# Optimization experiments

Measured on AMD Instinct MI355X. Metric: run time of the kernel, lower is better.

Reference implementation:

```python
import jax, jax.numpy as jnp
import numpy as np

DIM = 128
HID = 128
EPS = 1e-6  # flax nnx.LayerNorm default epsilon


def _layernorm(x, scale, bias):
    mu = jnp.mean(x, axis=-1, keepdims=True)
    var = jnp.mean(jnp.square(x - mu), axis=-1, keepdims=True)
    return (x - mu) * jax.lax.rsqrt(var + EPS) * scale + bias


def setup_inputs() -> dict:
    key = jax.random.key(0)
    ks = jax.random.split(key, 16)
    B, N = 1, 512
    s = 1.0 / np.sqrt(DIM)
    inp = {
        "x": jax.random.normal(ks[0], (B, N, N, DIM), dtype=jnp.float32),
        "src_mask": jnp.ones((B, N), dtype=jnp.float32),
        "norm_scale": jnp.ones((DIM,), jnp.float32),
        "norm_bias": jnp.zeros((DIM,), jnp.float32),
        "W_left": jax.random.normal(ks[1], (DIM, HID), jnp.float32) * s,
        "b_left": jnp.zeros((HID,), jnp.float32),
        "W_right": jax.random.normal(ks[2], (DIM, HID), jnp.float32) * s,
        "b_right": jnp.zeros((HID,), jnp.float32),
        "W_lgate": jax.random.normal(ks[3], (DIM, HID), jnp.float32) * s,
        "b_lgate": jnp.zeros((HID,), jnp.float32),
        "W_rgate": jax.random.normal(ks[4], (DIM, HID), jnp.float32) * s,
        "b_rgate": jnp.zeros((HID,), jnp.float32),
        "W_ogate": jax.random.normal(ks[5], (DIM, HID), jnp.float32) * s,
        "b_ogate": jnp.zeros((HID,), jnp.float32),
        "out_norm_scale": jnp.ones((HID,), jnp.float32),
        "out_norm_bias": jnp.zeros((HID,), jnp.float32),
        "W_out": jax.random.normal(ks[6], (HID, DIM), jnp.float32) * (1.0 / np.sqrt(HID)),
        "b_out": jnp.zeros((DIM,), jnp.float32),
    }
    return inp


def reference(x, src_mask, norm_scale, norm_bias, W_left, b_left, W_right, b_right,
              W_lgate, b_lgate, W_rgate, b_rgate, W_ogate, b_ogate,
              out_norm_scale, out_norm_bias, W_out, b_out):
    # pair mask [B,N,N,1] = outer product of token mask
    m = src_mask.astype(jnp.float32)
    mask = (m[:, :, None] * m[:, None, :])[..., None]

    xn = _layernorm(x, norm_scale, norm_bias)  # [B,N,N,D]

    left = (xn @ W_left + b_left) * mask
    right = (xn @ W_right + b_right) * mask
    left = left * jax.nn.sigmoid(xn @ W_lgate + b_lgate)
    right = right * jax.nn.sigmoid(xn @ W_rgate + b_rgate)
    out_gate = jax.nn.sigmoid(xn @ W_ogate + b_ogate)

    # ingoing mix: '... k i d, ... k j d -> ... i j d'
    out = jnp.einsum('bkid,bkjd->bijd', left, right)

    out = _layernorm(out, out_norm_scale, out_norm_bias) * out_gate
    return out @ W_out + b_out
```

## Files before the change

### kernel.cpp

```cpp
#include <hip/hip_runtime.h>


#define NN 512
#define DD 128
#define PT (NN * NN)

typedef float f4 __attribute__((ext_vector_type(4)));
typedef __bf16 bf8 __attribute__((ext_vector_type(8)));
typedef unsigned short u16;
typedef unsigned int u32;
typedef u16 us4 __attribute__((ext_vector_type(4)));
typedef u16 us8 __attribute__((ext_vector_type(8)));

__device__ __forceinline__ u16 f2bf(float f) {
    u32 u = __float_as_uint(f);
    return (u16)((u + 0x7fffu + ((u >> 16) & 1u)) >> 16);
}
__device__ __forceinline__ float bf2f(u16 h) { return __uint_as_float(((u32)h) << 16); }
__device__ __forceinline__ float sigm(float x) {
    return __builtin_amdgcn_rcpf(1.0f + __builtin_amdgcn_exp2f(-1.4426950408889634f * x));
}
__device__ __forceinline__ f4 mfma16(bf8 a, bf8 b, f4 c) {
    return __builtin_amdgcn_mfma_f32_16x16x32_bf16(a, b, c, 0, 0, 0);
}
__device__ __forceinline__ void async16(u16* lds, const u16* g) {
    __builtin_amdgcn_global_load_lds((const __attribute__((address_space(1))) u32*)(const void*)g,
                                     (__attribute__((address_space(3))) u32*)(void*)lds, 16, 0, 0);
}

__global__ __launch_bounds__(256) void kW(const float* __restrict__ wlg, const float* __restrict__ wl,
                                          const float* __restrict__ wrg, const float* __restrict__ wr,
                                          const float* __restrict__ wog, const float* __restrict__ wout,
                                          u16* __restrict__ wt, u16* __restrict__ wtout) {
    __shared__ float tile[128 * 129];
    const float* srcs[6] = {wlg, wl, wrg, wr, wog, wout};
    const int b = blockIdx.x;
    const float* s = srcs[b];
    u16* dst = (b < 5) ? (wt + b * 16384) : wtout;
    const int t = threadIdx.x;
    for (int idx = t; idx < 16384; idx += 256) {
        int k = idx >> 7, n = idx & 127;
        tile[k * 129 + n] = s[idx];
    }
    __syncthreads();
    for (int idx = t; idx < 16384; idx += 256) {
        int n = idx >> 7, k = idx & 127;
        dst[n * 128 + k] = f2bf(tile[k * 129 + n]);
    }
}

__global__ __launch_bounds__(256) void kA(const float* __restrict__ x, const float* __restrict__ smask,
                                          const float* __restrict__ nsc, const float* __restrict__ nbi,
                                          const float* __restrict__ b_l, const float* __restrict__ b_r,
                                          const float* __restrict__ b_lg, const float* __restrict__ b_rg,
                                          const float* __restrict__ b_og, const u16* __restrict__ wt,
                                          u16* __restrict__ left_v, u16* __restrict__ right_v,
                                          u16* __restrict__ gate) {
    __shared__ u16 xs[128 * 136];
    __shared__ float ns[128], nb[128], smk[128];
    u16* tmp = xs;

    const int t = threadIdx.x;
    const int bid = blockIdx.x;
    const int i_blk = bid & 511;
    const int k0 = (bid >> 9) << 7;

    if (t < 128) { ns[t] = nsc[t]; nb[t] = nbi[t]; smk[t] = smask[k0 + t]; }
    const float mi = smask[i_blk];
    __syncthreads();

    {
        const int rr = t >> 1, h = t & 1;
        const float* xr = x + ((long)(k0 + rr) * NN + i_blk) * DD + h * 64;
        f4 xv[16];
#pragma unroll
        for (int q = 0; q < 16; ++q) xv[q] = ((const f4*)xr)[q];
        float s = 0.f, ss = 0.f;
#pragma unroll
        for (int q = 0; q < 16; ++q)
#pragma unroll
            for (int e = 0; e < 4; ++e) { float f = xv[q][e]; s += f; ss += f * f; }
        s += __shfl_xor(s, 1); ss += __shfl_xor(ss, 1);
        const float mu = s * (1.f / 128.f);
        const float rstd = rsqrtf(ss * (1.f / 128.f) - mu * mu + 1e-6f);
        u16* xrow = xs + rr * 136 + h * 64;
#pragma unroll
        for (int q = 0; q < 16; ++q) {
            f4 sc = ((const f4*)ns)[h * 16 + q];
            f4 bi = ((const f4*)nb)[h * 16 + q];
            us4 pk;
#pragma unroll
            for (int e = 0; e < 4; ++e) pk[e] = f2bf((xv[q][e] - mu) * rstd * sc[e] + bi[e]);
            *(us4*)(xrow + q * 4) = pk;
        }
    }
    __syncthreads();

    const int lane = t & 63, w = t >> 6;
    const int m = lane & 15, q = lane >> 4;

    bf8 af[2][4];
#pragma unroll
    for (int st = 0; st < 2; ++st) {
        const int row = (w * 2 + st) * 16 + m;
#pragma unroll
        for (int kc = 0; kc < 4; ++kc) af[st][kc] = *(const bf8*)&xs[row * 136 + kc * 32 + q * 8];
    }
    __syncthreads();

#pragma unroll
    for (int g = 0; g < 3; ++g) {
        const u16* wg = wt + (g == 0 ? 0 : (g == 1 ? 2 * 16384 : 4 * 16384));
        const float* bg = (g == 0) ? b_lg : (g == 1 ? b_rg : b_og);
        f4 accG[16];
#pragma unroll
        for (int nt = 0; nt < 8; ++nt) {
            bf8 bfr[4];
#pragma unroll
            for (int kc = 0; kc < 4; ++kc)
                bfr[kc] = *(const bf8*)(wg + (nt * 16 + m) * 128 + kc * 32 + q * 8);
#pragma unroll
            for (int st = 0; st < 2; ++st) {
                f4 a = {0.f, 0.f, 0.f, 0.f};
#pragma unroll
                for (int kc = 0; kc < 4; ++kc) a = mfma16(af[st][kc], bfr[kc], a);
                accG[nt * 2 + st] = a;
            }
        }
        if (g < 2) {
            const u16* wv = wt + (g == 0 ? 1 : 3) * 16384;
            const float* bv = (g == 0) ? b_l : b_r;
#pragma unroll
            for (int nt = 0; nt < 8; ++nt) {
                bf8 bfr[4];
#pragma unroll
                for (int kc = 0; kc < 4; ++kc)
                    bfr[kc] = *(const bf8*)(wv + (nt * 16 + m) * 128 + kc * 32 + q * 8);
                const int d = nt * 16 + m;
                const float bvn = bv[d], bgn = bg[d];
#pragma unroll
                for (int st = 0; st < 2; ++st) {
                    f4 a = {0.f, 0.f, 0.f, 0.f};
#pragma unroll
                    for (int kc = 0; kc < 4; ++kc) a = mfma16(af[st][kc], bfr[kc], a);
                    const int rr0 = (w * 2 + st) * 16 + q * 4;
                    us4 pk;
#pragma unroll
                    for (int r = 0; r < 4; ++r) {
                        float gv = sigm(accG[nt * 2 + st][r] + bgn);
                        pk[r] = f2bf((a[r] + bvn) * (smk[rr0 + r] * mi) * gv);
                    }
                    *(us4*)&tmp[d * 136 + rr0] = pk;
                }
            }
        } else {
#pragma unroll
            for (int nt = 0; nt < 8; ++nt) {
                const int d = nt * 16 + m;
                const float bgn = bg[d];
#pragma unroll
                for (int st = 0; st < 2; ++st) {
                    const int rr0 = (w * 2 + st) * 16 + q * 4;
#pragma unroll
                    for (int r = 0; r < 4; ++r)
                        tmp[(rr0 + r) * 136 + d] = f2bf(sigm(accG[nt * 2 + st][r] + bgn));
                }
            }
        }
        __syncthreads();
        if (g < 2) {
            u16* dst = (g == 0) ? left_v : right_v;
#pragma unroll
            for (int r8 = 0; r8 < 8; ++r8) {
                const int d = (t >> 4) + r8 * 16;
                const int mc = t & 15;
                us8 vv = *(const us8*)&tmp[d * 136 + mc * 8];
                *(us8*)(dst + (long)d * PT + (long)i_blk * NN + k0 + mc * 8) = vv;
            }
        } else {
#pragma unroll
            for (int r8 = 0; r8 < 8; ++r8) {
                const int rrr = (t >> 4) + r8 * 16;
                const int dc = t & 15;
                us8 vv = *(const us8*)&tmp[rrr * 136 + dc * 8];
                *(us8*)(gate + ((long)(k0 + rrr) * NN + i_blk) * DD + dc * 8) = vv;
            }
        }
        __syncthreads();
    }
}

__global__ __launch_bounds__(256) void kB(const u16* __restrict__ left_v, const u16* __restrict__ right_v,
                                          u16* __restrict__ out_t) {
    __shared__ u16 smem[128 * 136];
    u16* As = smem;
    u16* Bs = smem + 4096;
    const int t = threadIdx.x, lane = t & 63, w = t >> 6;
    const int bid = blockIdx.x;
    const int d = bid >> 4;
    const int ti = (bid & 3) * 128;
    const int tj = ((bid >> 2) & 3) * 128;
    const long dbase = (long)d * PT;
    const int frow = lane >> 2;
    const int fc = (lane & 3) ^ ((lane >> 3) & 3);
    const int m = lane & 15, q = lane >> 4;
    const int sl = q ^ ((m >> 1) & 3);
    const int mrow0 = (w & 1) * 64;
    const int nrow0 = (w >> 1) * 64;

    f4 zero = {0.f, 0.f, 0.f, 0.f};
    f4 acc[16];
#pragma unroll
    for (int z = 0; z < 16; ++z) acc[z] = zero;

    const u16* Agb = left_v + dbase + (long)ti * NN;
    const u16* Bgb = right_v + dbase + (long)tj * NN;

    for (int ks = 0; ks < 16; ++ks) {
        __syncthreads();
#pragma unroll
        for (int inst = 0; inst < 2; ++inst) {
            const int rbase = w * 32 + inst * 16;
            const int row = rbase + frow;
            async16(As + rbase * 32, Agb + (long)row * NN + ks * 32 + fc * 8);
            async16(Bs + rbase * 32, Bgb + (long)row * NN + ks * 32 + fc * 8);
        }
        __syncthreads();
        bf8 af[4], bfv[4];
#pragma unroll
        for (int mt = 0; mt < 4; ++mt) af[mt] = *(const bf8*)&As[(mrow0 + mt * 16 + m) * 32 + sl * 8];
#pragma unroll
        for (int nt = 0; nt < 4; ++nt) bfv[nt] = *(const bf8*)&Bs[(nrow0 + nt * 16 + m) * 32 + sl * 8];
#pragma unroll
        for (int mt = 0; mt < 4; ++mt)
#pragma unroll
            for (int nt = 0; nt < 4; ++nt) acc[mt * 4 + nt] = mfma16(af[mt], bfv[nt], acc[mt * 4 + nt]);
    }
    __syncthreads();
    u16* ct = smem;
#pragma unroll
    for (int mt = 0; mt < 4; ++mt)
#pragma unroll
        for (int nt = 0; nt < 4; ++nt) {
            const int row0 = mrow0 + mt * 16 + q * 4;
            const int col = nrow0 + nt * 16 + m;
            f4 a = acc[mt * 4 + nt];
#pragma unroll
            for (int r = 0; r < 4; ++r) ct[(row0 + r) * 136 + col] = f2bf(a[r]);
        }
    __syncthreads();
#pragma unroll
    for (int r8 = 0; r8 < 8; ++r8) {
        const int row = (t >> 4) + r8 * 16;
        const int mc = t & 15;
        us8 vv = *(const us8*)&ct[row * 136 + mc * 8];
        *(us8*)(out_t + dbase + (long)(ti + row) * NN + tj + mc * 8) = vv;
    }
}

__global__ __launch_bounds__(256) void kC(const u16* __restrict__ out_t, const u16* __restrict__ gate,
                                          const float* __restrict__ osc_g, const float* __restrict__ obi_g,
                                          const u16* __restrict__ wtout, const float* __restrict__ b_out,
                                          float* __restrict__ out) {
    __shared__ u16 os[128 * 128];
    __shared__ float osc[128], obi[128];
    const int t = threadIdx.x;
    const int bid = blockIdx.x;
    const int i = bid >> 2;
    const int j0 = (bid & 3) * 128;
    if (t < 128) { osc[t] = osc_g[t]; obi[t] = obi_g[t]; }
    const long p0 = (long)i * NN + j0;

#pragma unroll
    for (int r8 = 0; r8 < 8; ++r8) {
        const int dd = (t >> 4) + r8 * 16;
        const int mm = t & 15;
        us8 vv = *(const us8*)(out_t + (long)dd * PT + (long)i * NN + j0 + mm * 8);
        const int cd = dd >> 3, dl = dd & 7;
#pragma unroll
        for (int e = 0; e < 8; ++e) {
            const int ee = e ^ (mm & 7);
            const int j = mm * 8 + ee;
            os[j * 128 + ((cd ^ (j & 15)) << 3) + dl] = vv[ee];
        }
    }
    __syncthreads();
    {
        const int j = t >> 1, h = t & 1;
        const long p = p0 + j;
        float s = 0.f, ss = 0.f;
#pragma unroll
        for (int cc = 0; cc < 8; ++cc) {
            const int cd = h * 8 + cc;
            us8 vv = *(const us8*)&os[j * 128 + ((cd ^ (j & 15)) << 3)];
#pragma unroll
            for (int e = 0; e < 8; ++e) { float f = bf2f(vv[e]); s += f; ss += f * f; }
        }
        s += __shfl_xor(s, 1); ss += __shfl_xor(ss, 1);
        const float mu = s * (1.f / 128.f);
        const float rstd = rsqrtf(ss * (1.f / 128.f) - mu * mu + 1e-6f);
#pragma unroll
        for (int cc = 0; cc < 8; ++cc) {
            const int cd = h * 8 + cc;
            u16* slotp = &os[j * 128 + ((cd ^ (j & 15)) << 3)];
            us8 vv = *(const us8*)slotp;
            us8 gv = *(const us8*)(gate + p * DD + cd * 8);
            us8 rv;
#pragma unroll
            for (int e = 0; e < 8; ++e) {
                const int d2 = cd * 8 + e;
                float f = (bf2f(vv[e]) - mu) * rstd * osc[d2] + obi[d2];
                rv[e] = f2bf(f * bf2f(gv[e]));
            }
            *(us8*)slotp = rv;
        }
    }
    __syncthreads();
    const int lane = t & 63, w = t >> 6;
    const int m = lane & 15, q = lane >> 4;
    bf8 af[2][4];
#pragma unroll
    for (int st = 0; st < 2; ++st) {
        const int jr = (w * 2 + st) * 16 + m;
#pragma unroll
        for (int kc = 0; kc < 4; ++kc) {
            const int cd = kc * 4 + q;
            af[st][kc] = *(const bf8*)&os[jr * 128 + ((cd ^ (jr & 15)) << 3)];
        }
    }
#pragma unroll
    for (int nt = 0; nt < 8; ++nt) {
        bf8 bfr[4];
#pragma unroll
        for (int kc = 0; kc < 4; ++kc)
            bfr[kc] = *(const bf8*)(wtout + (nt * 16 + m) * 128 + kc * 32 + q * 8);
        const float bo = b_out[nt * 16 + m];
#pragma unroll
        for (int st = 0; st < 2; ++st) {
            f4 a = {0.f, 0.f, 0.f, 0.f};
#pragma unroll
            for (int kc = 0; kc < 4; ++kc) a = mfma16(af[st][kc], bfr[kc], a);
            const int rr0 = (w * 2 + st) * 16 + q * 4;
#pragma unroll
            for (int r = 0; r < 4; ++r) out[(p0 + rr0 + r) * DD + nt * 16 + m] = a[r] + bo;
        }
    }
}

extern "C" void kernel_launch(void* const* d_in, const int* in_sizes, int n_in, void* d_out, int out_size,
                              void* d_ws, size_t ws_size, hipStream_t stream) {
    const float* x = (const float*)d_in[0];
    const float* sm = (const float*)d_in[1];
    const float* nsc = (const float*)d_in[2];
    const float* nbi = (const float*)d_in[3];
    const float* wl = (const float*)d_in[4];
    const float* bl = (const float*)d_in[5];
    const float* wr = (const float*)d_in[6];
    const float* br = (const float*)d_in[7];
    const float* wlg = (const float*)d_in[8];
    const float* blg = (const float*)d_in[9];
    const float* wrg = (const float*)d_in[10];
    const float* brg = (const float*)d_in[11];
    const float* wog = (const float*)d_in[12];
    const float* bog = (const float*)d_in[13];
    const float* onsc = (const float*)d_in[14];
    const float* onbi = (const float*)d_in[15];
    const float* wout = (const float*)d_in[16];
    const float* bout = (const float*)d_in[17];

    char* ws = (char*)d_ws;
    u16* wt = (u16*)ws;
    u16* wtout = (u16*)(ws + 163840);
    u16* left_v = (u16*)(ws + 262144);
    u16* right_v = left_v + (long)DD * PT;
    u16* gate = right_v + (long)DD * PT;
    u16* out_t = gate + (long)DD * PT;

    kW<<<6, 256, 0, stream>>>(wlg, wl, wrg, wr, wog, wout, wt, wtout);
    kA<<<2048, 256, 0, stream>>>(x, sm, nsc, nbi, bl, br, blg, brg, bog, wt, left_v, right_v, gate);
    kB<<<2048, 256, 0, stream>>>(left_v, right_v, out_t);
    kC<<<2048, 256, 0, stream>>>(out_t, gate, onsc, onbi, wtout, bout, (float*)d_out);
}
```

Measured before the change: 582.4 us.

## Stage LayerNorm input via async global-to-LDS loads and build MFMA fragments directly

Each wave loads its x rows into swizzled fp32 LDS staging with async 16-byte copies, in two 16-row rounds. It computes LayerNorm stats with 4 lanes per row and writes the normalized bf16 A-fragments straight into registers. This drops the bf16 LDS round trip and one barrier, and it hides global latency behind async copies. The cost is a serialized second load round per wave, plus extra shuffles and waitcnt handling.

Result: no change. 575.8 us (-1.1%).

```diff
diff --git a/kernel.cpp b/kernel.cpp
--- a/kernel.cpp
+++ b/kernel.cpp
@@ -59,52 +59,77 @@
     __shared__ u16 xs[128 * 136];
     __shared__ float ns[128], nb[128], smk[128];
     u16* tmp = xs;
+    float* stg = (float*)xs;
 
     const int t = threadIdx.x;
     const int bid = blockIdx.x;
     const int i_blk = bid & 511;
     const int k0 = (bid >> 9) << 7;
+    const int lane = t & 63, w = t >> 6;
+    const int m = lane & 15, q = lane >> 4;
 
     if (t < 128) { ns[t] = nsc[t]; nb[t] = nbi[t]; smk[t] = smask[k0 + t]; }
     const float mi = smask[i_blk];
-    __syncthreads();
-
-    {
-        const int rr = t >> 1, h = t & 1;
-        const float* xr = x + ((long)(k0 + rr) * NN + i_blk) * DD + h * 64;
-        f4 xv[16];
-#pragma unroll
-        for (int q = 0; q < 16; ++q) xv[q] = ((const f4*)xr)[q];
+
+#pragma unroll
+    for (int it = 0; it < 8; ++it) {
+        const int rl = it * 2 + (lane >> 5);
+        const int c = (lane & 31) ^ (rl & 7);
+        const float* gp = x + ((long)(k0 + w * 32 + rl) * NN + i_blk) * DD + c * 4;
+        async16((u16*)(stg + w * 2048 + it * 256), (const u16*)gp);
+    }
+
+    bf8 af[2][4];
+#pragma unroll
+    for (int rd = 0; rd < 2; ++rd) {
+        if (rd == 0) {
+            __syncthreads();
+        } else {
+            asm volatile("s_waitcnt lgkmcnt(0)" ::: "memory");
+            __builtin_amdgcn_sched_barrier(0);
+#pragma unroll
+            for (int it = 0; it < 8; ++it) {
+                const int rl = it * 2 + (lane >> 5);
+                const int c = (lane & 31) ^ (rl & 7);
+                const float* gp = x + ((long)(k0 + w * 32 + 16 + rl) * NN + i_blk) * DD + c * 4;
+                async16((u16*)(stg + w * 2048 + it * 256), (const u16*)gp);
+            }
+            asm volatile("s_waitcnt vmcnt(0)" ::: "memory");
+            __builtin_amdgcn_sched_barrier(0);
+        }
+        const float* wbase = stg + w * 2048;
+        const int rl_s = lane >> 2, h2 = lane & 3;
         float s = 0.f, ss = 0.f;
-#pragma unroll
-        for (int q = 0; q < 16; ++q)
-#pragma unroll
-            for (int e = 0; e < 4; ++e) { float f = xv[q][e]; s += f; ss += f * f; }
+        f4 vv[8];
+#pragma unroll
+        for (int q2 = 0; q2 < 8; ++q2)
+            vv[q2] = ((const f4*)(wbase + rl_s * 128))[(h2 * 8 + q2) ^ (rl_s & 7)];
+#pragma unroll
+        for (int q2 = 0; q2 < 8; ++q2)
+#pragma unroll
+            for (int e = 0; e < 4; ++e) { float f = vv[q2][e]; s += f; ss += f * f; }
         s += __shfl_xor(s, 1); ss += __shfl_xor(ss, 1);
+        s += __shfl_xor(s, 2); ss += __shfl_xor(ss, 2);
         const float mu = s * (1.f / 128.f);
         const float rstd = rsqrtf(ss * (1.f / 128.f) - mu * mu + 1e-6f);
-        u16* xrow = xs + rr * 136 + h * 64;
-#pragma unroll
-        for (int q = 0; q < 16; ++q) {
-            f4 sc = ((const f4*)ns)[h * 16 + q];
-            f4 bi = ((const f4*)nb)[h * 16 + q];
-            us4 pk;
-#pragma unroll
-            for (int e = 0; e < 4; ++e) pk[e] = f2bf((xv[q][e] - mu) * rstd * sc[e] + bi[e]);
-            *(us4*)(xrow + q * 4) = pk;
-        }
-    }
-    __syncthreads();
-
-    const int lane = t & 63, w = t >> 6;
-    const int m = lane & 15, q = lane >> 4;
-
-    bf8 af[2][4];
-#pragma unroll
-    for (int st = 0; st < 2; ++st) {
-        const int row = (w * 2 + st) * 16 + m;
-#pragma unroll
-        for (int kc = 0; kc < 4; ++kc) af[st][kc] = *(const bf8*)&xs[row * 136 + kc * 32 + q * 8];
+        const float muM = __shfl(mu, m << 2);
+        const float rsM = __shfl(rstd, m << 2);
+#pragma unroll
+        for (int kc = 0; kc < 4; ++kc) {
+            const int c0 = kc * 8 + q * 2;
+            const f4* rowp = (const f4*)(wbase + m * 128);
+            f4 x0 = rowp[c0 ^ (m & 7)];
+            f4 x1 = rowp[(c0 + 1) ^ (m & 7)];
+            f4 s0 = ((const f4*)ns)[c0], s1 = ((const f4*)ns)[c0 + 1];
+            f4 b0 = ((const f4*)nb)[c0], b1 = ((const f4*)nb)[c0 + 1];
+            us8 pk;
+#pragma unroll
+            for (int e = 0; e < 4; ++e) {
+                pk[e] = f2bf((x0[e] - muM) * rsM * s0[e] + b0[e]);
+                pk[e + 4] = f2bf((x1[e] - muM) * rsM * s1[e] + b1[e]);
+            }
+            af[rd][kc] = *(const bf8*)&pk;
+        }
     }
     __syncthreads();
 
```

## Split input LayerNorm into separate kernel writing bf16 normalized activations

Applied to the files above, without the earlier changes.

Moves the first LayerNorm out of the projection kernel into a new kernel that reads x contiguously and writes bf16 normalized rows into a scratch buffer that aliases the later out_t buffer. The projection kernel then loads half-size bf16 rows with a strided pattern instead of strided fp32 rows. This is meant to make the fp32 read of x coalesced and to shrink the strided traffic. The cost is an extra kernel launch plus a full write and re-read of a 64 MB intermediate.

New measurement: 600.9 us. 1.03x slower.

```diff
diff --git a/kernel.cpp b/kernel.cpp
--- a/kernel.cpp
+++ b/kernel.cpp
@@ -49,15 +49,57 @@
     }
 }
 
-__global__ __launch_bounds__(256) void kA(const float* __restrict__ x, const float* __restrict__ smask,
-                                          const float* __restrict__ nsc, const float* __restrict__ nbi,
+__global__ __launch_bounds__(256) void kN(const float* __restrict__ x, const float* __restrict__ nsc,
+                                          const float* __restrict__ nbi, u16* __restrict__ xn) {
+    __shared__ float ns[128], nb[128];
+    const int t = threadIdx.x;
+    if (t < 128) { ns[t] = nsc[t]; nb[t] = nbi[t]; }
+    __syncthreads();
+    const long p0 = (long)blockIdx.x * 128;
+    const int rloc = t >> 3;
+    const int c = t & 7;
+#pragma unroll
+    for (int pass = 0; pass < 4; ++pass) {
+        const long p = p0 + pass * 32 + rloc;
+        const float* xr = x + p * DD + c * 16;
+        f4 xv[4];
+#pragma unroll
+        for (int q = 0; q < 4; ++q) xv[q] = ((const f4*)xr)[q];
+        float s = 0.f, ss = 0.f;
+#pragma unroll
+        for (int q = 0; q < 4; ++q)
+#pragma unroll
+            for (int e = 0; e < 4; ++e) { float f = xv[q][e]; s += f; ss += f * f; }
+        s += __shfl_xor(s, 1); ss += __shfl_xor(ss, 1);
+        s += __shfl_xor(s, 2); ss += __shfl_xor(ss, 2);
+        s += __shfl_xor(s, 4); ss += __shfl_xor(ss, 4);
+        const float mu = s * (1.f / 128.f);
+        const float rstd = rsqrtf(ss * (1.f / 128.f) - mu * mu + 1e-6f);
+        us8 o0, o1;
+#pragma unroll
+        for (int q = 0; q < 4; ++q) {
+            f4 sc = ((const f4*)ns)[c * 4 + q];
+            f4 bi = ((const f4*)nb)[c * 4 + q];
+#pragma unroll
+            for (int e = 0; e < 4; ++e) {
+                u16 v = f2bf((xv[q][e] - mu) * rstd * sc[e] + bi[e]);
+                if (q < 2) o0[q * 4 + e] = v; else o1[(q - 2) * 4 + e] = v;
+            }
+        }
+        u16* orow = xn + p * DD + c * 16;
+        *(us8*)orow = o0;
+        *(us8*)(orow + 8) = o1;
+    }
+}
+
+__global__ __launch_bounds__(256) void kA(const u16* __restrict__ xn, const float* __restrict__ smask,
                                           const float* __restrict__ b_l, const float* __restrict__ b_r,
                                           const float* __restrict__ b_lg, const float* __restrict__ b_rg,
                                           const float* __restrict__ b_og, const u16* __restrict__ wt,
                                           u16* __restrict__ left_v, u16* __restrict__ right_v,
                                           u16* __restrict__ gate) {
     __shared__ u16 xs[128 * 136];
-    __shared__ float ns[128], nb[128], smk[128];
+    __shared__ float smk[128];
     u16* tmp = xs;
 
     const int t = threadIdx.x;
@@ -65,34 +107,16 @@
     const int i_blk = bid & 511;
     const int k0 = (bid >> 9) << 7;
 
-    if (t < 128) { ns[t] = nsc[t]; nb[t] = nbi[t]; smk[t] = smask[k0 + t]; }
+    if (t < 128) smk[t] = smask[k0 + t];
     const float mi = smask[i_blk];
-    __syncthreads();
-
-    {
-        const int rr = t >> 1, h = t & 1;
-        const float* xr = x + ((long)(k0 + rr) * NN + i_blk) * DD + h * 64;
-        f4 xv[16];
-#pragma unroll
-        for (int q = 0; q < 16; ++q) xv[q] = ((const f4*)xr)[q];
-        float s = 0.f, ss = 0.f;
-#pragma unroll
-        for (int q = 0; q < 16; ++q)
-#pragma unroll
-            for (int e = 0; e < 4; ++e) { float f = xv[q][e]; s += f; ss += f * f; }
-        s += __shfl_xor(s, 1); ss += __shfl_xor(ss, 1);
-        const float mu = s * (1.f / 128.f);
-        const float rstd = rsqrtf(ss * (1.f / 128.f) - mu * mu + 1e-6f);
-        u16* xrow = xs + rr * 136 + h * 64;
-#pragma unroll
-        for (int q = 0; q < 16; ++q) {
-            f4 sc = ((const f4*)ns)[h * 16 + q];
-            f4 bi = ((const f4*)nb)[h * 16 + q];
-            us4 pk;
-#pragma unroll
-            for (int e = 0; e < 4; ++e) pk[e] = f2bf((xv[q][e] - mu) * rstd * sc[e] + bi[e]);
-            *(us4*)(xrow + q * 4) = pk;
-        }
+
+#pragma unroll
+    for (int c8 = 0; c8 < 8; ++c8) {
+        const int row = (t >> 4) + c8 * 16;
+        const int ch = t & 15;
+        const long p = (long)(k0 + row) * NN + i_blk;
+        us8 v = *(const us8*)(xn + p * DD + ch * 8);
+        *(us8*)&xs[row * 136 + ch * 8] = v;
     }
     __syncthreads();
 
@@ -375,9 +399,11 @@
     u16* right_v = left_v + (long)DD * PT;
     u16* gate = right_v + (long)DD * PT;
     u16* out_t = gate + (long)DD * PT;
+    u16* xn = out_t;
 
     kW<<<6, 256, 0, stream>>>(wlg, wl, wrg, wr, wog, wout, wt, wtout);
-    kA<<<2048, 256, 0, stream>>>(x, sm, nsc, nbi, bl, br, blg, brg, bog, wt, left_v, right_v, gate);
+    kN<<<2048, 256, 0, stream>>>(x, nsc, nbi, xn);
+    kA<<<2048, 256, 0, stream>>>(xn, sm, bl, br, blg, brg, bog, wt, left_v, right_v, gate);
     kB<<<2048, 256, 0, stream>>>(left_v, right_v, out_t);
     kC<<<2048, 256, 0, stream>>>(out_t, gate, onsc, onbi, wtout, bout, (float*)d_out);
 }
```

## Read x contiguously in projection kernel and add separate transpose kernels

Applied to the files above, without the earlier changes.

The projection kernel now processes contiguous 128-row blocks of x in natural (k,i,d) order and writes left/right in natural layout instead of scattering directly into per-channel planes. Two new transpose kernels then convert left and right into the d-plane layout the einsum kernel expects, reusing workspace buffers. This is meant to remove the strided global reads and scattered writes in the projection kernel. The cost is an extra read and write of both 64MB bf16 tensors plus two more kernel launches.

Result: slower. 662.8 us (+13.8%).

```diff
diff --git a/kernel.cpp b/kernel.cpp
--- a/kernel.cpp
+++ b/kernel.cpp
@@ -54,24 +54,25 @@
                                           const float* __restrict__ b_l, const float* __restrict__ b_r,
                                           const float* __restrict__ b_lg, const float* __restrict__ b_rg,
                                           const float* __restrict__ b_og, const u16* __restrict__ wt,
-                                          u16* __restrict__ left_v, u16* __restrict__ right_v,
+                                          u16* __restrict__ left_n, u16* __restrict__ right_n,
                                           u16* __restrict__ gate) {
     __shared__ u16 xs[128 * 136];
-    __shared__ float ns[128], nb[128], smk[128];
+    __shared__ float ns[128], nb[128], smi[128];
     u16* tmp = xs;
 
     const int t = threadIdx.x;
     const int bid = blockIdx.x;
-    const int i_blk = bid & 511;
-    const int k0 = (bid >> 9) << 7;
-
-    if (t < 128) { ns[t] = nsc[t]; nb[t] = nbi[t]; smk[t] = smask[k0 + t]; }
-    const float mi = smask[i_blk];
+    const long p0 = (long)bid * 128;
+    const int kk = bid >> 2;
+    const int i0 = (bid & 3) * 128;
+    const float mk = smask[kk];
+
+    if (t < 128) { ns[t] = nsc[t]; nb[t] = nbi[t]; smi[t] = smask[i0 + t]; }
     __syncthreads();
 
     {
         const int rr = t >> 1, h = t & 1;
-        const float* xr = x + ((long)(k0 + rr) * NN + i_blk) * DD + h * 64;
+        const float* xr = x + (p0 + rr) * DD + h * 64;
         f4 xv[16];
 #pragma unroll
         for (int q = 0; q < 16; ++q) xv[q] = ((const f4*)xr)[q];
@@ -99,6 +100,12 @@
     const int lane = t & 63, w = t >> 6;
     const int m = lane & 15, q = lane >> 4;
 
+    float simr[2][4];
+#pragma unroll
+    for (int st = 0; st < 2; ++st)
+#pragma unroll
+        for (int r = 0; r < 4; ++r) simr[st][r] = smi[(w * 2 + st) * 16 + q * 4 + r] * mk;
+
     bf8 af[2][4];
 #pragma unroll
     for (int st = 0; st < 2; ++st) {
@@ -144,13 +151,11 @@
 #pragma unroll
                     for (int kc = 0; kc < 4; ++kc) a = mfma16(af[st][kc], bfr[kc], a);
                     const int rr0 = (w * 2 + st) * 16 + q * 4;
-                    us4 pk;
 #pragma unroll
                     for (int r = 0; r < 4; ++r) {
                         float gv = sigm(accG[nt * 2 + st][r] + bgn);
-                        pk[r] = f2bf((a[r] + bvn) * (smk[rr0 + r] * mi) * gv);
+                        tmp[(rr0 + r) * 136 + d] = f2bf((a[r] + bvn) * simr[st][r] * gv);
                     }
-                    *(us4*)&tmp[d * 136 + rr0] = pk;
                 }
             }
         } else {
@@ -168,25 +173,47 @@
             }
         }
         __syncthreads();
-        if (g < 2) {
-            u16* dst = (g == 0) ? left_v : right_v;
-#pragma unroll
-            for (int r8 = 0; r8 < 8; ++r8) {
-                const int d = (t >> 4) + r8 * 16;
-                const int mc = t & 15;
-                us8 vv = *(const us8*)&tmp[d * 136 + mc * 8];
-                *(us8*)(dst + (long)d * PT + (long)i_blk * NN + k0 + mc * 8) = vv;
-            }
-        } else {
+        {
+            u16* dst = (g == 0) ? left_n : (g == 1 ? right_n : gate);
 #pragma unroll
             for (int r8 = 0; r8 < 8; ++r8) {
                 const int rrr = (t >> 4) + r8 * 16;
                 const int dc = t & 15;
                 us8 vv = *(const us8*)&tmp[rrr * 136 + dc * 8];
-                *(us8*)(gate + ((long)(k0 + rrr) * NN + i_blk) * DD + dc * 8) = vv;
+                *(us8*)(dst + (p0 + rrr) * DD + dc * 8) = vv;
             }
         }
         __syncthreads();
+    }
+}
+
+__global__ __launch_bounds__(256) void kT(const u16* __restrict__ nat, u16* __restrict__ dplane) {
+    __shared__ u16 ld[32 * 520];
+    const int t = threadIdx.x;
+    const int bid = blockIdx.x;
+    const int i = bid >> 2;
+    const int d0 = (bid & 3) * 32;
+
+#pragma unroll
+    for (int half = 0; half < 2; ++half) {
+        const int k = half * 256 + t;
+        const u16* src = nat + ((long)k * NN + i) * DD + d0;
+        us8 v[4];
+#pragma unroll
+        for (int c = 0; c < 4; ++c) v[c] = ((const us8*)src)[c];
+#pragma unroll
+        for (int c = 0; c < 4; ++c)
+#pragma unroll
+            for (int e = 0; e < 8; ++e) ld[(c * 8 + e) * 520 + k] = v[c][e];
+    }
+    __syncthreads();
+#pragma unroll
+    for (int r = 0; r < 8; ++r) {
+        const int idx = r * 256 + t;
+        const int dl = idx >> 6;
+        const int g = idx & 63;
+        us8 v = *(const us8*)&ld[dl * 520 + g * 8];
+        *(us8*)(dplane + (long)(d0 + dl) * PT + (long)i * NN + g * 8) = v;
     }
 }
 
@@ -371,13 +398,15 @@
     char* ws = (char*)d_ws;
     u16* wt = (u16*)ws;
     u16* wtout = (u16*)(ws + 163840);
-    u16* left_v = (u16*)(ws + 262144);
-    u16* right_v = left_v + (long)DD * PT;
-    u16* gate = right_v + (long)DD * PT;
-    u16* out_t = gate + (long)DD * PT;
+    u16* S1 = (u16*)(ws + 262144);
+    u16* S2 = S1 + (long)DD * PT;
+    u16* S3 = S2 + (long)DD * PT;
+    u16* S4 = S3 + (long)DD * PT;
 
     kW<<<6, 256, 0, stream>>>(wlg, wl, wrg, wr, wog, wout, wt, wtout);
-    kA<<<2048, 256, 0, stream>>>(x, sm, nsc, nbi, bl, br, blg, brg, bog, wt, left_v, right_v, gate);
-    kB<<<2048, 256, 0, stream>>>(left_v, right_v, out_t);
-    kC<<<2048, 256, 0, stream>>>(out_t, gate, onsc, onbi, wtout, bout, (float*)d_out);
-}
+    kA<<<2048, 256, 0, stream>>>(x, sm, nsc, nbi, bl, br, blg, brg, bog, wt, S1, S2, S3);
+    kT<<<2048, 256, 0, stream>>>(S1, S4);
+    kT<<<2048, 256, 0, stream>>>(S2, S1);
+    kB<<<2048, 256, 0, stream>>>(S4, S1, S2);
+    kC<<<2048, 256, 0, stream>>>(S2, S3, onsc, onbi, wtout, bout, (float*)d_out);
+}
```
